# Kernel tuning notes

Hardware: AMD Instinct MI355X
Metric: run time of the kernel (lower is better)

The kernel has to match this reference:

```python
import jax, jax.numpy as jnp
import numpy as np

ALPHA = 0.2  # LeakyReLU negative slope
MASK_VAL = -9e15


def setup_inputs() -> dict:
    key = jax.random.key(0)
    k1, k2, k3, k4 = jax.random.split(key, 4)
    N, F_in, F_out = 8192, 512, 128
    h = jax.random.normal(k1, (N, F_in), dtype=jnp.float32)
    adj = jax.random.randint(k2, (N, N), 0, 2, dtype=jnp.int32)
    w = jax.random.normal(k3, (F_in, F_out), dtype=jnp.float32) * 0.05
    a = jax.random.normal(k4, (2 * F_out, 1), dtype=jnp.float32) * 0.05
    return {"h": h, "adj": adj, "w": w, "a": a}


def reference(h, adj, w, a):
    F_out = w.shape[1]
    Wh = h @ w                                  # [N, F_out]
    Wh1 = Wh @ a[:F_out, :]                     # [N, 1]
    Wh2 = Wh @ a[F_out:, :]                     # [N, 1]
    e = Wh1 + Wh2.T                             # [N, N] broadcast additive score
    e = jnp.where(e > 0, e, ALPHA * e)          # LeakyReLU
    att = jnp.where(adj > 0, e, MASK_VAL)       # mask non-edges
    att = jax.nn.softmax(att, axis=1)           # row softmax
    # dropout is identity in eval mode
    h_prime = att @ Wh                          # [N, F_out]
    return jax.nn.elu(h_prime)                  # concat=True -> ELU
```

## Files before the change

### kernel.cpp

```cpp
#include <hip/hip_runtime.h>
#include <hip/hip_bf16.h>

#define LRELU_ALPHA 0.2f

constexpr int N   = 8192;
constexpr int FIN = 512;
constexpr int F   = 128;
constexpr int BRW = 16;
constexpr int BR  = 64;
constexpr int BK  = 64;

typedef __attribute__((ext_vector_type(4))) float f32x4;
typedef __attribute__((ext_vector_type(8))) short s16x8;
typedef __attribute__((ext_vector_type(4))) short s16x4;
typedef __attribute__((ext_vector_type(4))) int   i32x4;

static __device__ __forceinline__ short f2bf(float x) {
  unsigned u = __float_as_uint(x);
  return (short)((u + 0x7fffu + ((u >> 16) & 1u)) >> 16);
}

__global__ __launch_bounds__(256) void k_wh(
    const float* __restrict__ h, const float* __restrict__ w,
    const float* __restrict__ a, __hip_bfloat16* __restrict__ WhbT,
    float* __restrict__ Wh1, float* __restrict__ Wh2) {
  __shared__ float hl[32][68];
  __shared__ float wl[64][128];
  const int t    = threadIdx.x;
  const int i0   = blockIdx.x * 32;
  const int col4 = (t & 31) * 4;
  const int rq   = t >> 5;
  float acc[4][4] = {};

  for (int k0 = 0; k0 < FIN; k0 += 64) {
#pragma unroll
    for (int j = 0; j < 2; ++j) {
      int c = t + 256 * j;
      int r = c >> 4, kq = c & 15;
      *(f32x4*)&hl[r][kq * 4] =
          *(const f32x4*)(h + (size_t)(i0 + r) * FIN + k0 + kq * 4);
    }
#pragma unroll
    for (int j = 0; j < 8; ++j) {
      int c = t + 256 * j;
      int kr = c >> 5, f4 = (c & 31) * 4;
      *(f32x4*)&wl[kr][f4] = *(const f32x4*)(w + (size_t)(k0 + kr) * F + f4);
    }
    __syncthreads();
#pragma unroll 4
    for (int k4 = 0; k4 < 64; k4 += 4) {
      f32x4 wv[4];
#pragma unroll
      for (int u = 0; u < 4; ++u) wv[u] = *(const f32x4*)&wl[k4 + u][col4];
#pragma unroll
      for (int ri = 0; ri < 4; ++ri) {
        f32x4 hv = *(const f32x4*)&hl[rq * 4 + ri][k4];
#pragma unroll
        for (int u = 0; u < 4; ++u) {
#pragma unroll
          for (int ci = 0; ci < 4; ++ci) acc[ri][ci] += hv[u] * wv[u][ci];
        }
      }
    }
    __syncthreads();
  }
#pragma unroll
  for (int ci = 0; ci < 4; ++ci) {
    int f = col4 + ci;
    s16x4 o = {f2bf(acc[0][ci]), f2bf(acc[1][ci]),
               f2bf(acc[2][ci]), f2bf(acc[3][ci])};
    *(s16x4*)((short*)WhbT + (size_t)f * N + i0 + rq * 4) = o;
  }
  f32x4 av1 = *(const f32x4*)(a + col4);
  f32x4 av2 = *(const f32x4*)(a + F + col4);
  float s1[4], s2[4];
#pragma unroll
  for (int ri = 0; ri < 4; ++ri) {
    s1[ri] = acc[ri][0] * av1[0] + acc[ri][1] * av1[1] +
             acc[ri][2] * av1[2] + acc[ri][3] * av1[3];
    s2[ri] = acc[ri][0] * av2[0] + acc[ri][1] * av2[1] +
             acc[ri][2] * av2[2] + acc[ri][3] * av2[3];
  }
#pragma unroll
  for (int off = 1; off < 32; off <<= 1) {
#pragma unroll
    for (int ri = 0; ri < 4; ++ri) {
      s1[ri] += __shfl_xor(s1[ri], off);
      s2[ri] += __shfl_xor(s2[ri], off);
    }
  }
  if ((t & 31) == 0) {
#pragma unroll
    for (int ri = 0; ri < 4; ++ri) {
      Wh1[i0 + rq * 4 + ri] = s1[ri];
      Wh2[i0 + rq * 4 + ri] = s2[ri];
    }
  }
}

template <int KS>
__global__ __launch_bounds__(256) __attribute__((amdgpu_waves_per_eu(1, 4)))
void k_attn(
    const int* __restrict__ adj, const float* __restrict__ Wh1v,
    const float* __restrict__ Wh2v, const __hip_bfloat16* __restrict__ WhbT,
    float* __restrict__ accP, float* __restrict__ lP) {
  constexpr int JW  = N / KS;
  constexpr int NTL = JW / BK;
  __shared__ __align__(16) short Bl[2][F * BK];

  const int t   = threadIdx.x;
  const int l   = t & 63;
  const int w   = t >> 6;
  const int r16 = l & 15;
  const int g8  = (l >> 4) * 8;
  const int i0  = blockIdx.x * BR;
  const int s   = blockIdx.y;

  const int row  = i0 + w * BRW + r16;
  const float w1 = Wh1v[row];
  const int* __restrict__ rowp   = adj + (size_t)row * N + (size_t)s * JW;
  const float* __restrict__ w2p  = Wh2v + (size_t)s * JW;
  const short* __restrict__ bsrc = (const short*)WhbT + (size_t)s * JW;

  int ldsoff[4]; size_t goff[4];
#pragma unroll
  for (int q = 0; q < 4; ++q) {
    int c  = t + 256 * q;
    int fr = c >> 3;
    ldsoff[q] = (c * 16) ^ ((fr & 7) << 4);
    goff[q]   = (size_t)fr * N + (c & 7) * 8;
  }
  const int sw = (r16 & 7) << 4;

  f32x4 acc[8] = {};
  float lsum = 0.f;
  s16x8 sv[4];

  i32x4 aA0, aA1, aA2, aA3, aB0, aB1, aB2, aB3;
  f32x4 cA0, cA1, cA2, cA3, cB0, cB1, cB2, cB3;

#define LOAD_SCORE(A0, A1, A2, A3, C0, C1, C2, C3, off)                      \
  A0 = *(const i32x4*)(rowp + (off) + g8);                                   \
  A1 = *(const i32x4*)(rowp + (off) + g8 + 4);                               \
  A2 = *(const i32x4*)(rowp + (off) + g8 + 32);                              \
  A3 = *(const i32x4*)(rowp + (off) + g8 + 36);                              \
  C0 = *(const f32x4*)(w2p + (off) + g8);                                    \
  C1 = *(const f32x4*)(w2p + (off) + g8 + 4);                                \
  C2 = *(const f32x4*)(w2p + (off) + g8 + 32);                               \
  C3 = *(const f32x4*)(w2p + (off) + g8 + 36);

  auto scores = [&](const i32x4& x0, const i32x4& x1, const i32x4& x2,
                    const i32x4& x3, const f32x4& y0, const f32x4& y1,
                    const f32x4& y2, const f32x4& y3, s16x8& af0, s16x8& af1) {
    float p[16];
#pragma unroll
    for (int u = 0; u < 4; ++u) {
      float x = w1 + y0[u]; x = fmaxf(x, LRELU_ALPHA * x);
      p[u] = x0[u] > 0 ? __expf(x) : 0.f;
    }
#pragma unroll
    for (int u = 0; u < 4; ++u) {
      float x = w1 + y1[u]; x = fmaxf(x, LRELU_ALPHA * x);
      p[4 + u] = x1[u] > 0 ? __expf(x) : 0.f;
    }
#pragma unroll
    for (int u = 0; u < 4; ++u) {
      float x = w1 + y2[u]; x = fmaxf(x, LRELU_ALPHA * x);
      p[8 + u] = x2[u] > 0 ? __expf(x) : 0.f;
    }
#pragma unroll
    for (int u = 0; u < 4; ++u) {
      float x = w1 + y3[u]; x = fmaxf(x, LRELU_ALPHA * x);
      p[12 + u] = x3[u] > 0 ? __expf(x) : 0.f;
    }
#pragma unroll
    for (int u = 0; u < 16; ++u) lsum += p[u];
    af0 = s16x8{f2bf(p[0]),  f2bf(p[1]),  f2bf(p[2]),  f2bf(p[3]),
                f2bf(p[4]),  f2bf(p[5]),  f2bf(p[6]),  f2bf(p[7])};
    af1 = s16x8{f2bf(p[8]),  f2bf(p[9]),  f2bf(p[10]), f2bf(p[11]),
                f2bf(p[12]), f2bf(p[13]), f2bf(p[14]), f2bf(p[15])};
  };

  auto mfma_tile = [&](const char* pb, s16x8 af0, s16x8 af1) {
#pragma unroll
    for (int nb = 0; nb < 8; ++nb) {
      const int rbase = (nb * 16 + r16) * 128;
      s16x8 b0 = *(const s16x8*)(pb + rbase + ((g8 * 2) ^ sw));
      s16x8 b1 = *(const s16x8*)(pb + rbase + ((g8 * 2 + 64) ^ sw));
      acc[nb] = __builtin_amdgcn_mfma_f32_16x16x32_bf16(af0, b0, acc[nb], 0, 0, 0);
      acc[nb] = __builtin_amdgcn_mfma_f32_16x16x32_bf16(af1, b1, acc[nb], 0, 0, 0);
    }
  };

#pragma unroll
  for (int q = 0; q < 4; ++q) sv[q] = *(const s16x8*)(bsrc + goff[q]);
  LOAD_SCORE(aA0, aA1, aA2, aA3, cA0, cA1, cA2, cA3, 0)
  LOAD_SCORE(aB0, aB1, aB2, aB3, cB0, cB1, cB2, cB3, BK)
#pragma unroll
  for (int q = 0; q < 4; ++q)
    *(s16x8*)((char*)&Bl[0][0] + ldsoff[q]) = sv[q];
  __syncthreads();

  for (int tl = 0; tl < NTL; tl += 2) {
    {
      const size_t tn = (size_t)(tl + 1 < NTL ? tl + 1 : NTL - 1) * BK;
#pragma unroll
      for (int q = 0; q < 4; ++q)
        sv[q] = *(const s16x8*)(bsrc + goff[q] + tn);
    }
    {
      s16x8 af0, af1;
      scores(aA0, aA1, aA2, aA3, cA0, cA1, cA2, cA3, af0, af1);
      const int tp = (tl + 2 < NTL ? tl + 2 : tl) * BK;
      LOAD_SCORE(aA0, aA1, aA2, aA3, cA0, cA1, cA2, cA3, tp)
#pragma unroll
      for (int q = 0; q < 4; ++q)
        *(s16x8*)((char*)&Bl[1][0] + ldsoff[q]) = sv[q];
      mfma_tile((const char*)&Bl[0][0], af0, af1);
    }
    __syncthreads();
    {
      const size_t tn = (size_t)(tl + 2 < NTL ? tl + 2 : NTL - 1) * BK;
#pragma unroll
      for (int q = 0; q < 4; ++q)
        sv[q] = *(const s16x8*)(bsrc + goff[q] + tn);
    }
    {
      s16x8 af0, af1;
      scores(aB0, aB1, aB2, aB3, cB0, cB1, cB2, cB3, af0, af1);
      const int tp = (tl + 3 < NTL ? tl + 3 : tl + 1) * BK;
      LOAD_SCORE(aB0, aB1, aB2, aB3, cB0, cB1, cB2, cB3, tp)
#pragma unroll
      for (int q = 0; q < 4; ++q)
        *(s16x8*)((char*)&Bl[0][0] + ldsoff[q]) = sv[q];
      mfma_tile((const char*)&Bl[1][0], af0, af1);
    }
    __syncthreads();
  }
#undef LOAD_SCORE

  lsum += __shfl_xor(lsum, 16);
  lsum += __shfl_xor(lsum, 32);
  if (l < 16) lP[(size_t)s * N + row] = lsum;
  float* op = accP + (size_t)s * N * F;
#pragma unroll
  for (int nb = 0; nb < 8; ++nb) {
#pragma unroll
    for (int rg = 0; rg < 4; ++rg) {
      int r = i0 + w * BRW + (l >> 4) * 4 + rg;
      op[(size_t)r * F + nb * 16 + r16] = acc[nb][rg];
    }
  }
}

template <int KS>
__global__ __launch_bounds__(256) void k_comb(
    const float* __restrict__ accP, const float* __restrict__ lP,
    float* __restrict__ out) {
  const int idx = blockIdx.x * 256 + threadIdx.x;
  const int i   = idx >> 5;
  f32x4 v = {};
  float lt = 0.f;
#pragma unroll
  for (int s = 0; s < KS; ++s) {
    v += *(const f32x4*)(accP + (size_t)s * N * F + (size_t)idx * 4);
    lt += lP[(size_t)s * N + i];
  }
  f32x4 o;
#pragma unroll
  for (int u = 0; u < 4; ++u) {
    float x = v[u] / lt;
    o[u] = x > 0.f ? x : __expf(x) - 1.f;
  }
  *(f32x4*)(out + (size_t)idx * 4) = o;
}

extern "C" void kernel_launch(void* const* d_in, const int* in_sizes, int n_in,
                              void* d_out, int out_size, void* d_ws, size_t ws_size,
                              hipStream_t stream) {
  const float* h   = (const float*)d_in[0];
  const int*   adj = (const int*)d_in[1];
  const float* w   = (const float*)d_in[2];
  const float* a   = (const float*)d_in[3];
  float* out = (float*)d_out;

  char* ws = (char*)d_ws;
  __hip_bfloat16* WhbT = (__hip_bfloat16*)ws;
  float* Wh1 = (float*)(ws + (size_t)F * N * 2);
  float* Wh2 = Wh1 + N;
  float* lP  = Wh2 + N;

  const size_t fixed = (size_t)F * N * 2 + 2 * (size_t)N * 4;
  const size_t need8 = fixed + 8 * (size_t)N * 4 + 8 * (size_t)N * F * 4;

  k_wh<<<N / 32, 256, 0, stream>>>(h, w, a, WhbT, Wh1, Wh2);
  if (ws_size >= need8) {
    constexpr int KS = 8;
    float* accP = lP + (size_t)KS * N;
    k_attn<KS><<<dim3(N / BR, KS), 256, 0, stream>>>(adj, Wh1, Wh2, WhbT,
                                                     accP, lP);
    k_comb<KS><<<(N * F / 4) / 256, 256, 0, stream>>>(accP, lP, out);
  } else {
    constexpr int KS = 4;
    float* accP = lP + (size_t)KS * N;
    k_attn<KS><<<dim3(N / BR, KS), 256, 0, stream>>>(adj, Wh1, Wh2, WhbT,
                                                     accP, lP);
    k_comb<KS><<<(N * F / 4) / 256, 256, 0, stream>>>(accP, lP, out);
  }
}
```

Before: 130.7 us.

## Pack adjacency into per-row bitmasks in a prepass kernel before attention

Adds a k_mask kernel that streams the int32 adjacency matrix once and packs it into 64-bit ballot bitmasks, one bit per edge. The attention kernel then reads one u64 per 64-column tile instead of 64 int32 values, and tests edges by bit-shifting. The aim is to take the heavy adjacency stream out of the MFMA/exp loop so that loop is no longer slowed by adjacency load latency. In exchange it adds an extra launch, an 8 MB mask buffer in workspace, and a separate pass whose speed is bound by the adjacency read.

```diff
diff --git a/kernel.cpp b/kernel.cpp
--- a/kernel.cpp
+++ b/kernel.cpp
@@ -9,15 +9,42 @@
 constexpr int BRW = 16;
 constexpr int BR  = 64;
 constexpr int BK  = 64;
+constexpr int NW64 = N / 64;
 
 typedef __attribute__((ext_vector_type(4))) float f32x4;
 typedef __attribute__((ext_vector_type(8))) short s16x8;
 typedef __attribute__((ext_vector_type(4))) short s16x4;
 typedef __attribute__((ext_vector_type(4))) int   i32x4;
+typedef unsigned long long u64;
 
 static __device__ __forceinline__ short f2bf(float x) {
   unsigned u = __float_as_uint(x);
   return (short)((u + 0x7fffu + ((u >> 16) & 1u)) >> 16);
+}
+
+__global__ __launch_bounds__(256) void k_mask(
+    const int* __restrict__ adj, u64* __restrict__ mask) {
+  const int l   = threadIdx.x & 63;
+  const int row = blockIdx.x * 4 + (threadIdx.x >> 6);
+  const int* __restrict__ rp = adj + (size_t)row * N;
+  u64* __restrict__ mp = mask + (size_t)row * NW64;
+  for (int it = 0; it < N / 512; ++it) {
+    const int base = it * 512 + l;
+    int v[8];
+#pragma unroll
+    for (int k = 0; k < 8; ++k) v[k] = rp[base + k * 64];
+    u64 m[8];
+#pragma unroll
+    for (int k = 0; k < 8; ++k) m[k] = __ballot(v[k] > 0);
+    if (l == 0) {
+      ulonglong2 s0 = {m[0], m[1]}, s1 = {m[2], m[3]};
+      ulonglong2 s2 = {m[4], m[5]}, s3 = {m[6], m[7]};
+      *(ulonglong2*)(mp + it * 8)     = s0;
+      *(ulonglong2*)(mp + it * 8 + 2) = s1;
+      *(ulonglong2*)(mp + it * 8 + 4) = s2;
+      *(ulonglong2*)(mp + it * 8 + 6) = s3;
+    }
+  }
 }
 
 __global__ __launch_bounds__(256) void k_wh(
@@ -101,7 +128,7 @@
 template <int KS>
 __global__ __launch_bounds__(256) __attribute__((amdgpu_waves_per_eu(1, 4)))
 void k_attn(
-    const int* __restrict__ adj, const float* __restrict__ Wh1v,
+    const u64* __restrict__ mask, const float* __restrict__ Wh1v,
     const float* __restrict__ Wh2v, const __hip_bfloat16* __restrict__ WhbT,
     float* __restrict__ accP, float* __restrict__ lP) {
   constexpr int JW  = N / KS;
@@ -118,7 +145,7 @@
 
   const int row  = i0 + w * BRW + r16;
   const float w1 = Wh1v[row];
-  const int* __restrict__ rowp   = adj + (size_t)row * N + (size_t)s * JW;
+  const u64* __restrict__ mrow   = mask + (size_t)row * NW64 + s * (JW / 64);
   const float* __restrict__ w2p  = Wh2v + (size_t)s * JW;
   const short* __restrict__ bsrc = (const short*)WhbT + (size_t)s * JW;
 
@@ -136,42 +163,40 @@
   float lsum = 0.f;
   s16x8 sv[4];
 
-  i32x4 aA0, aA1, aA2, aA3, aB0, aB1, aB2, aB3;
+  u64 mA, mB;
   f32x4 cA0, cA1, cA2, cA3, cB0, cB1, cB2, cB3;
 
-#define LOAD_SCORE(A0, A1, A2, A3, C0, C1, C2, C3, off)                      \
-  A0 = *(const i32x4*)(rowp + (off) + g8);                                   \
-  A1 = *(const i32x4*)(rowp + (off) + g8 + 4);                               \
-  A2 = *(const i32x4*)(rowp + (off) + g8 + 32);                              \
-  A3 = *(const i32x4*)(rowp + (off) + g8 + 36);                              \
-  C0 = *(const f32x4*)(w2p + (off) + g8);                                    \
-  C1 = *(const f32x4*)(w2p + (off) + g8 + 4);                                \
-  C2 = *(const f32x4*)(w2p + (off) + g8 + 32);                               \
-  C3 = *(const f32x4*)(w2p + (off) + g8 + 36);
-
-  auto scores = [&](const i32x4& x0, const i32x4& x1, const i32x4& x2,
-                    const i32x4& x3, const f32x4& y0, const f32x4& y1,
+#define LOAD_SCORE(M, C0, C1, C2, C3, tile)                                  \
+  M  = mrow[(tile)];                                                         \
+  C0 = *(const f32x4*)(w2p + (tile) * BK + g8);                              \
+  C1 = *(const f32x4*)(w2p + (tile) * BK + g8 + 4);                          \
+  C2 = *(const f32x4*)(w2p + (tile) * BK + g8 + 32);                         \
+  C3 = *(const f32x4*)(w2p + (tile) * BK + g8 + 36);
+
+  auto scores = [&](u64 m, const f32x4& y0, const f32x4& y1,
                     const f32x4& y2, const f32x4& y3, s16x8& af0, s16x8& af1) {
+    const unsigned b0 = (unsigned)(m >> g8) & 0xffu;
+    const unsigned b1 = (unsigned)(m >> (g8 + 32)) & 0xffu;
     float p[16];
 #pragma unroll
     for (int u = 0; u < 4; ++u) {
       float x = w1 + y0[u]; x = fmaxf(x, LRELU_ALPHA * x);
-      p[u] = x0[u] > 0 ? __expf(x) : 0.f;
+      p[u] = (b0 >> u) & 1u ? __expf(x) : 0.f;
     }
 #pragma unroll
     for (int u = 0; u < 4; ++u) {
       float x = w1 + y1[u]; x = fmaxf(x, LRELU_ALPHA * x);
-      p[4 + u] = x1[u] > 0 ? __expf(x) : 0.f;
+      p[4 + u] = (b0 >> (4 + u)) & 1u ? __expf(x) : 0.f;
     }
 #pragma unroll
     for (int u = 0; u < 4; ++u) {
       float x = w1 + y2[u]; x = fmaxf(x, LRELU_ALPHA * x);
-      p[8 + u] = x2[u] > 0 ? __expf(x) : 0.f;
+      p[8 + u] = (b1 >> u) & 1u ? __expf(x) : 0.f;
     }
 #pragma unroll
     for (int u = 0; u < 4; ++u) {
       float x = w1 + y3[u]; x = fmaxf(x, LRELU_ALPHA * x);
-      p[12 + u] = x3[u] > 0 ? __expf(x) : 0.f;
+      p[12 + u] = (b1 >> (4 + u)) & 1u ? __expf(x) : 0.f;
     }
 #pragma unroll
     for (int u = 0; u < 16; ++u) lsum += p[u];
@@ -194,8 +219,8 @@
 
 #pragma unroll
   for (int q = 0; q < 4; ++q) sv[q] = *(const s16x8*)(bsrc + goff[q]);
-  LOAD_SCORE(aA0, aA1, aA2, aA3, cA0, cA1, cA2, cA3, 0)
-  LOAD_SCORE(aB0, aB1, aB2, aB3, cB0, cB1, cB2, cB3, BK)
+  LOAD_SCORE(mA, cA0, cA1, cA2, cA3, 0)
+  LOAD_SCORE(mB, cB0, cB1, cB2, cB3, 1)
 #pragma unroll
   for (int q = 0; q < 4; ++q)
     *(s16x8*)((char*)&Bl[0][0] + ldsoff[q]) = sv[q];
@@ -210,9 +235,9 @@
     }
     {
       s16x8 af0, af1;
-      scores(aA0, aA1, aA2, aA3, cA0, cA1, cA2, cA3, af0, af1);
-      const int tp = (tl + 2 < NTL ? tl + 2 : tl) * BK;
-      LOAD_SCORE(aA0, aA1, aA2, aA3, cA0, cA1, cA2, cA3, tp)
+      scores(mA, cA0, cA1, cA2, cA3, af0, af1);
+      const int tp = (tl + 2 < NTL ? tl + 2 : tl);
+      LOAD_SCORE(mA, cA0, cA1, cA2, cA3, tp)
 #pragma unroll
       for (int q = 0; q < 4; ++q)
         *(s16x8*)((char*)&Bl[1][0] + ldsoff[q]) = sv[q];
@@ -227,9 +252,9 @@
     }
     {
       s16x8 af0, af1;
-      scores(aB0, aB1, aB2, aB3, cB0, cB1, cB2, cB3, af0, af1);
-      const int tp = (tl + 3 < NTL ? tl + 3 : tl + 1) * BK;
-      LOAD_SCORE(aB0, aB1, aB2, aB3, cB0, cB1, cB2, cB3, tp)
+      scores(mB, cB0, cB1, cB2, cB3, af0, af1);
+      const int tp = (tl + 3 < NTL ? tl + 3 : tl + 1);
+      LOAD_SCORE(mB, cB0, cB1, cB2, cB3, tp)
 #pragma unroll
       for (int q = 0; q < 4; ++q)
         *(s16x8*)((char*)&Bl[0][0] + ldsoff[q]) = sv[q];
@@ -288,22 +313,25 @@
   __hip_bfloat16* WhbT = (__hip_bfloat16*)ws;
   float* Wh1 = (float*)(ws + (size_t)F * N * 2);
   float* Wh2 = Wh1 + N;
-  float* lP  = Wh2 + N;
-
-  const size_t fixed = (size_t)F * N * 2 + 2 * (size_t)N * 4;
+  u64*  mask = (u64*)(Wh2 + N);
+  float* lP  = (float*)(mask + (size_t)N * NW64);
+
+  const size_t fixed = (size_t)F * N * 2 + 2 * (size_t)N * 4 +
+                       (size_t)N * NW64 * 8;
   const size_t need8 = fixed + 8 * (size_t)N * 4 + 8 * (size_t)N * F * 4;
 
+  k_mask<<<N / 4, 256, 0, stream>>>(adj, mask);
   k_wh<<<N / 32, 256, 0, stream>>>(h, w, a, WhbT, Wh1, Wh2);
   if (ws_size >= need8) {
     constexpr int KS = 8;
     float* accP = lP + (size_t)KS * N;
-    k_attn<KS><<<dim3(N / BR, KS), 256, 0, stream>>>(adj, Wh1, Wh2, WhbT,
+    k_attn<KS><<<dim3(N / BR, KS), 256, 0, stream>>>(mask, Wh1, Wh2, WhbT,
                                                      accP, lP);
     k_comb<KS><<<(N * F / 4) / 256, 256, 0, stream>>>(accP, lP, out);
   } else {
     constexpr int KS = 4;
     float* accP = lP + (size_t)KS * N;
-    k_attn<KS><<<dim3(N / BR, KS), 256, 0, stream>>>(adj, Wh1, Wh2, WhbT,
+    k_attn<KS><<<dim3(N / BR, KS), 256, 0, stream>>>(mask, Wh1, Wh2, WhbT,
                                                      accP, lP);
     k_comb<KS><<<(N * F / 4) / 256, 256, 0, stream>>>(accP, lP, out);
   }
```

New measurement: 143.3 us. 9.6% more time.

## Preload adjacency tile as LDS bitmasks via ballot before the MFMA loop

Applied to the files above, without the earlier changes.

Before the main loop, each block streams its whole adjacency slab with coalesced loads, compresses it into 64-bit ballot masks stored in shared memory (XOR-swizzled), and also stages the Wh2 slice in LDS. The score lambda then reads mask bits and Wh2 from LDS instead of issuing per-tile global int loads inside the pipelined loop. This aims to turn the adjacency read into a fully coalesced bulk read and remove register pressure from the prefetched score operands. In exchange, the adjacency read is no longer overlapped with the MFMA work and LDS usage grows, which may lower occupancy.

```diff
diff --git a/kernel.cpp b/kernel.cpp
--- a/kernel.cpp
+++ b/kernel.cpp
@@ -14,6 +14,7 @@
 typedef __attribute__((ext_vector_type(8))) short s16x8;
 typedef __attribute__((ext_vector_type(4))) short s16x4;
 typedef __attribute__((ext_vector_type(4))) int   i32x4;
+typedef unsigned long long u64;
 
 static __device__ __forceinline__ short f2bf(float x) {
   unsigned u = __float_as_uint(x);
@@ -107,6 +108,8 @@
   constexpr int JW  = N / KS;
   constexpr int NTL = JW / BK;
   __shared__ __align__(16) short Bl[2][F * BK];
+  __shared__ u64   ml[BR][NTL];
+  __shared__ float w2l[JW];
 
   const int t   = threadIdx.x;
   const int l   = t & 63;
@@ -118,7 +121,6 @@
 
   const int row  = i0 + w * BRW + r16;
   const float w1 = Wh1v[row];
-  const int* __restrict__ rowp   = adj + (size_t)row * N + (size_t)s * JW;
   const float* __restrict__ w2p  = Wh2v + (size_t)s * JW;
   const short* __restrict__ bsrc = (const short*)WhbT + (size_t)s * JW;
 
@@ -136,42 +138,65 @@
   float lsum = 0.f;
   s16x8 sv[4];
 
-  i32x4 aA0, aA1, aA2, aA3, aB0, aB1, aB2, aB3;
-  f32x4 cA0, cA1, cA2, cA3, cB0, cB1, cB2, cB3;
-
-#define LOAD_SCORE(A0, A1, A2, A3, C0, C1, C2, C3, off)                      \
-  A0 = *(const i32x4*)(rowp + (off) + g8);                                   \
-  A1 = *(const i32x4*)(rowp + (off) + g8 + 4);                               \
-  A2 = *(const i32x4*)(rowp + (off) + g8 + 32);                              \
-  A3 = *(const i32x4*)(rowp + (off) + g8 + 36);                              \
-  C0 = *(const f32x4*)(w2p + (off) + g8);                                    \
-  C1 = *(const f32x4*)(w2p + (off) + g8 + 4);                                \
-  C2 = *(const f32x4*)(w2p + (off) + g8 + 32);                               \
-  C3 = *(const f32x4*)(w2p + (off) + g8 + 36);
-
-  auto scores = [&](const i32x4& x0, const i32x4& x1, const i32x4& x2,
-                    const i32x4& x3, const f32x4& y0, const f32x4& y1,
-                    const f32x4& y2, const f32x4& y3, s16x8& af0, s16x8& af1) {
+#pragma unroll
+  for (int q = 0; q < 4; ++q) sv[q] = *(const s16x8*)(bsrc + goff[q]);
+
+  if (t * 4 < JW) *(f32x4*)&w2l[t * 4] = *(const f32x4*)(w2p + t * 4);
+
+  {
+    const int* __restrict__ ap = adj + (size_t)(i0 + w * BRW) * N +
+                                 (size_t)s * JW;
+    for (int r = 0; r < BRW; ++r) {
+      const int* __restrict__ rp = ap + (size_t)r * N;
+#pragma unroll
+      for (int it = 0; it < JW / 512; ++it) {
+        int v[8];
+#pragma unroll
+        for (int k = 0; k < 8; ++k) v[k] = rp[it * 512 + l + k * 64];
+        u64 m[8];
+#pragma unroll
+        for (int k = 0; k < 8; ++k) m[k] = __ballot(v[k] > 0);
+        if (l == 0) {
+#pragma unroll
+          for (int k = 0; k < 8; ++k)
+            ml[w * BRW + r][(it * 8 + k) ^ r] = m[k];
+        }
+      }
+    }
+  }
+#pragma unroll
+  for (int q = 0; q < 4; ++q)
+    *(s16x8*)((char*)&Bl[0][0] + ldsoff[q]) = sv[q];
+  __syncthreads();
+
+  auto scores = [&](int tl, s16x8& af0, s16x8& af1) {
+    const u64 m = ml[w * BRW + r16][tl ^ r16];
+    const f32x4 y0 = *(const f32x4*)&w2l[tl * BK + g8];
+    const f32x4 y1 = *(const f32x4*)&w2l[tl * BK + g8 + 4];
+    const f32x4 y2 = *(const f32x4*)&w2l[tl * BK + g8 + 32];
+    const f32x4 y3 = *(const f32x4*)&w2l[tl * BK + g8 + 36];
+    const unsigned b0 = (unsigned)(m >> g8) & 0xffu;
+    const unsigned b1 = (unsigned)(m >> (g8 + 32)) & 0xffu;
     float p[16];
 #pragma unroll
     for (int u = 0; u < 4; ++u) {
       float x = w1 + y0[u]; x = fmaxf(x, LRELU_ALPHA * x);
-      p[u] = x0[u] > 0 ? __expf(x) : 0.f;
+      p[u] = (b0 >> u) & 1u ? __expf(x) : 0.f;
     }
 #pragma unroll
     for (int u = 0; u < 4; ++u) {
       float x = w1 + y1[u]; x = fmaxf(x, LRELU_ALPHA * x);
-      p[4 + u] = x1[u] > 0 ? __expf(x) : 0.f;
+      p[4 + u] = (b0 >> (4 + u)) & 1u ? __expf(x) : 0.f;
     }
 #pragma unroll
     for (int u = 0; u < 4; ++u) {
       float x = w1 + y2[u]; x = fmaxf(x, LRELU_ALPHA * x);
-      p[8 + u] = x2[u] > 0 ? __expf(x) : 0.f;
+      p[8 + u] = (b1 >> u) & 1u ? __expf(x) : 0.f;
     }
 #pragma unroll
     for (int u = 0; u < 4; ++u) {
       float x = w1 + y3[u]; x = fmaxf(x, LRELU_ALPHA * x);
-      p[12 + u] = x3[u] > 0 ? __expf(x) : 0.f;
+      p[12 + u] = (b1 >> (4 + u)) & 1u ? __expf(x) : 0.f;
     }
 #pragma unroll
     for (int u = 0; u < 16; ++u) lsum += p[u];
@@ -192,27 +217,14 @@
     }
   };
 
-#pragma unroll
-  for (int q = 0; q < 4; ++q) sv[q] = *(const s16x8*)(bsrc + goff[q]);
-  LOAD_SCORE(aA0, aA1, aA2, aA3, cA0, cA1, cA2, cA3, 0)
-  LOAD_SCORE(aB0, aB1, aB2, aB3, cB0, cB1, cB2, cB3, BK)
-#pragma unroll
-  for (int q = 0; q < 4; ++q)
-    *(s16x8*)((char*)&Bl[0][0] + ldsoff[q]) = sv[q];
-  __syncthreads();
-
   for (int tl = 0; tl < NTL; tl += 2) {
     {
-      const size_t tn = (size_t)(tl + 1 < NTL ? tl + 1 : NTL - 1) * BK;
+      const size_t tn = (size_t)(tl + 1) * BK;
 #pragma unroll
       for (int q = 0; q < 4; ++q)
         sv[q] = *(const s16x8*)(bsrc + goff[q] + tn);
-    }
-    {
       s16x8 af0, af1;
-      scores(aA0, aA1, aA2, aA3, cA0, cA1, cA2, cA3, af0, af1);
-      const int tp = (tl + 2 < NTL ? tl + 2 : tl) * BK;
-      LOAD_SCORE(aA0, aA1, aA2, aA3, cA0, cA1, cA2, cA3, tp)
+      scores(tl, af0, af1);
 #pragma unroll
       for (int q = 0; q < 4; ++q)
         *(s16x8*)((char*)&Bl[1][0] + ldsoff[q]) = sv[q];
@@ -220,16 +232,12 @@
     }
     __syncthreads();
     {
-      const size_t tn = (size_t)(tl + 2 < NTL ? tl + 2 : NTL - 1) * BK;
+      const size_t tn = (size_t)(tl + 2 < NTL ? tl + 2 : tl) * BK;
 #pragma unroll
       for (int q = 0; q < 4; ++q)
         sv[q] = *(const s16x8*)(bsrc + goff[q] + tn);
-    }
-    {
       s16x8 af0, af1;
-      scores(aB0, aB1, aB2, aB3, cB0, cB1, cB2, cB3, af0, af1);
-      const int tp = (tl + 3 < NTL ? tl + 3 : tl + 1) * BK;
-      LOAD_SCORE(aB0, aB1, aB2, aB3, cB0, cB1, cB2, cB3, tp)
+      scores(tl + 1, af0, af1);
 #pragma unroll
       for (int q = 0; q < 4; ++q)
         *(s16x8*)((char*)&Bl[0][0] + ldsoff[q]) = sv[q];
@@ -237,7 +245,6 @@
     }
     __syncthreads();
   }
-#undef LOAD_SCORE
 
   lsum += __shfl_xor(lsum, 16);
   lsum += __shfl_xor(lsum, 32);
```

After: 132.9 us. No clear change (+1.7%).
